# Optimization experiments

Measured on AMD Instinct MI355X. Metric: run time of the kernel, lower is better.

Reference implementation:

```python
import jax, jax.numpy as jnp
import numpy as np

# bitsandbytes NF4 codebook (16 levels, normalized to [-1, 1])
NF4_CODE = jnp.array([
    -1.0, -0.6961928009986877, -0.5250730514526367, -0.39491748809814453,
    -0.28444138169288635, -0.18477343022823334, -0.09105003625154495, 0.0,
    0.07958029955625534, 0.16093020141124725, 0.24611230194568634,
    0.33791524171829224, 0.44070982933044434, 0.5626170039176941,
    0.7229568362236023, 1.0], dtype=jnp.float32)

BLOCK = 64  # bitsandbytes default quantization blocksize
TOK, DIN, DOUT, RANK = 8192, 4096, 4096, 16
LORA_ALPHA = 16
SCALING = LORA_ALPHA / RANK ** 0.5  # rslora


def setup_inputs() -> dict:
    key = jax.random.key(0)
    k1, k2, k3, k4, k5, k6 = jax.random.split(key, 6)
    x = jax.random.normal(k1, (TOK, DIN), dtype=jnp.float32)
    w_codes = jax.random.randint(k2, (DOUT, DIN), 0, 16, dtype=jnp.int32)
    absmax = jax.random.uniform(k3, (DOUT, DIN // BLOCK), dtype=jnp.float32)
    bias = jax.random.normal(k4, (DOUT,), dtype=jnp.float32)
    lora_A = jax.random.normal(k5, (DIN, RANK), dtype=jnp.float32) * (1.0 / DIN ** 0.5)
    lora_B = jax.random.normal(k6, (RANK, DOUT), dtype=jnp.float32) * 0.02
    return {"x": x, "w_codes": w_codes, "absmax": absmax, "bias": bias,
            "lora_A": lora_A, "lora_B": lora_B}


def reference(x, w_codes, absmax, bias, lora_A, lora_B):
    # Dequantize NF4 base weight: codebook lookup * per-block absmax scale
    # W: [DOUT, DIN], absmax broadcast over blocks of 64 along DIN
    W = NF4_CODE[w_codes] * jnp.repeat(absmax, BLOCK, axis=1)
    base_out = x @ W.T + bias                      # [TOK, DOUT]
    lora_out = (x @ lora_A) @ lora_B               # low-rank path [TOK, DOUT]
    return base_out + lora_out * SCALING
```

## Files before the change

kernel.cpp:

```cpp
#include <hip/hip_runtime.h>
#include <hip/hip_bf16.h>
#include <cstdint>
#include <cstddef>

#define TOK   8192
#define DIN   4096
#define DOUT  4096
#define RANK  16
#define KE    4128

#define BM 256
#define BN 256
#define BKT 32
#define NKT (KE / BKT)
#define NBUF 3

typedef __attribute__((ext_vector_type(8))) short bf16x8;
typedef __attribute__((ext_vector_type(4))) float f32x4;
typedef __attribute__((ext_vector_type(8))) unsigned short u16x8;

__device__ __constant__ float NF4_CODE_D[16] = {
    -1.0f, -0.6961928009986877f, -0.5250730514526367f, -0.39491748809814453f,
    -0.28444138169288635f, -0.18477343022823334f, -0.09105003625154495f, 0.0f,
    0.07958029955625534f, 0.16093020141124725f, 0.24611230194568634f,
    0.33791524171829224f, 0.44070982933044434f, 0.5626170039176941f,
    0.7229568362236023f, 1.0f};

__device__ __forceinline__ unsigned short f2bf(float f) {
    union { float f; unsigned u; } v; v.f = f;
    unsigned u = v.u;
    unsigned r = (u + 0x7FFFu + ((u >> 16) & 1u)) >> 16;
    return (unsigned short)r;
}

__device__ __forceinline__ void async_copy16(const void* g, void* l) {
    __builtin_amdgcn_global_load_lds(
        (const __attribute__((address_space(1))) void*)g,
        (__attribute__((address_space(3))) void*)l,
        16, 0, 0);
}

__global__ __launch_bounds__(256) void prep_x(const float* __restrict__ x,
                                              const float* __restrict__ lora_A,
                                              unsigned short* __restrict__ xe) {
    const int tid = threadIdx.x;
    const int l = tid & 63;
    const int w = tid >> 6;
    const int t0 = blockIdx.x * 16 + w * 4;

    float p[4][16];
#pragma unroll
    for (int a = 0; a < 4; ++a)
#pragma unroll
        for (int r = 0; r < 16; ++r) p[a][r] = 0.f;

    for (int it = 0; it < 16; ++it) {
        const int kb = it * 256 + l * 4;
        float4 xv[4];
#pragma unroll
        for (int a = 0; a < 4; ++a)
            xv[a] = *(const float4*)(x + (size_t)(t0 + a) * DIN + kb);
#pragma unroll
        for (int a = 0; a < 4; ++a) {
            ushort4 s;
            s.x = f2bf(xv[a].x); s.y = f2bf(xv[a].y);
            s.z = f2bf(xv[a].z); s.w = f2bf(xv[a].w);
            *(ushort4*)(xe + (size_t)(t0 + a) * KE + kb) = s;
        }
#pragma unroll
        for (int j = 0; j < 4; ++j) {
            const float4* ap = (const float4*)(lora_A + (size_t)(kb + j) * RANK);
            const float4 a0 = ap[0], a1 = ap[1], a2 = ap[2], a3 = ap[3];
            const float av[16] = {a0.x, a0.y, a0.z, a0.w, a1.x, a1.y, a1.z, a1.w,
                                  a2.x, a2.y, a2.z, a2.w, a3.x, a3.y, a3.z, a3.w};
#pragma unroll
            for (int a = 0; a < 4; ++a) {
                const float xs = (j == 0) ? xv[a].x : (j == 1) ? xv[a].y
                                : (j == 2) ? xv[a].z : xv[a].w;
#pragma unroll
                for (int r = 0; r < 16; ++r) p[a][r] += xs * av[r];
            }
        }
    }

#pragma unroll
    for (int a = 0; a < 4; ++a) {
#pragma unroll
        for (int r = 0; r < 16; ++r) {
            float v = p[a][r];
#pragma unroll
            for (int off = 32; off > 0; off >>= 1) v += __shfl_xor(v, off, 64);
            if (l == r)
                xe[(size_t)(t0 + a) * KE + DIN + r] = f2bf(4.0f * v);
        }
        if (l >= 16 && l < 32)
            xe[(size_t)(t0 + a) * KE + DIN + l] =
                (l == 16) ? (unsigned short)0x3F80u : (unsigned short)0u;
    }
}

__global__ __launch_bounds__(256) void dequant_w(const int* __restrict__ codes,
                                                 const float* __restrict__ absmax,
                                                 unsigned short* __restrict__ we) {
    __shared__ float tab[16];
    if (threadIdx.x < 16) tab[threadIdx.x] = NF4_CODE_D[threadIdx.x];
    __syncthreads();
    const size_t tid = (size_t)blockIdx.x * 256 + threadIdx.x;
    const size_t base = tid * 8;
    const int o = (int)(base >> 12);
    const int k = (int)(base & (DIN - 1));
    const float am = absmax[base >> 6];
    const int4 c0 = *(const int4*)(codes + base);
    const int4 c1 = *(const int4*)(codes + base + 4);
    u16x8 ov;
    ov[0] = f2bf(tab[c0.x] * am);
    ov[1] = f2bf(tab[c0.y] * am);
    ov[2] = f2bf(tab[c0.z] * am);
    ov[3] = f2bf(tab[c0.w] * am);
    ov[4] = f2bf(tab[c1.x] * am);
    ov[5] = f2bf(tab[c1.y] * am);
    ov[6] = f2bf(tab[c1.z] * am);
    ov[7] = f2bf(tab[c1.w] * am);
    *(u16x8*)(we + (size_t)o * KE + k) = ov;
}

__global__ __launch_bounds__(256) void fill_wtail(const float* __restrict__ lora_B,
                                                  const float* __restrict__ bias,
                                                  unsigned short* __restrict__ we) {
    const int o = blockIdx.x * 256 + threadIdx.x;
    if (o >= DOUT) return;
    unsigned short* dst = we + (size_t)o * KE + DIN;
#pragma unroll
    for (int r = 0; r < RANK; ++r) dst[r] = f2bf(lora_B[(size_t)r * DOUT + o]);
    dst[16] = f2bf(bias[o]);
#pragma unroll
    for (int r = 17; r < 32; ++r) dst[r] = 0;
}

__global__ __launch_bounds__(512, 2) void gemm_bt(const unsigned short* __restrict__ A,
                                                  const unsigned short* __restrict__ B,
                                                  float* __restrict__ C) {
    __shared__ __attribute__((aligned(1024))) char smem[NBUF * 32768];

    const int tid = threadIdx.x;
    const int l = tid & 63;
    const int w = tid >> 6;
    const int wm = w >> 2;
    const int wn = w & 3;

    const int tm = blockIdx.x >> 4;
    const int tn = blockIdx.x & 15;
    const int rowBase = tm * BM;
    const int colBase = tn * BN;

    int srow[2], scolb[2], loffs[2];
#pragma unroll
    for (int g = 0; g < 2; ++g) {
        const int loff = g * 8192 + tid * 16;
        const int soff = loff ^ (((loff >> 7) & 7) << 4);
        loffs[g] = loff;
        srow[g] = soff >> 6;
        scolb[g] = soff & 63;
    }

    auto stage = [&](int t) {
        char* Ad = smem + (t % NBUF) * 32768;
        char* Bd = Ad + 16384;
        const int k0 = t * BKT;
#pragma unroll
        for (int g = 0; g < 2; ++g)
            async_copy16((const char*)A + ((size_t)(rowBase + srow[g]) * KE + k0) * 2 + scolb[g],
                         Ad + loffs[g]);
#pragma unroll
        for (int g = 0; g < 2; ++g)
            async_copy16((const char*)B + ((size_t)(colBase + srow[g]) * KE + k0) * 2 + scolb[g],
                         Bd + loffs[g]);
    };

    const int lmask = ((l >> 1) & 7) << 4;
    const int aoff = (((wm * 128 + (l & 15)) * 64) + ((l >> 4) * 16)) ^ lmask;
    const int boff = (((wn * 64 + (l & 15)) * 64) + ((l >> 4) * 16)) ^ lmask;

    f32x4 acc[8][4];
#pragma unroll
    for (int m = 0; m < 8; ++m)
#pragma unroll
        for (int n = 0; n < 4; ++n) acc[m][n] = (f32x4){0.f, 0.f, 0.f, 0.f};

    stage(0);
    stage(1);

    for (int t = 0; t < NKT; ++t) {
        if (t < NKT - 1) {
            asm volatile("s_waitcnt vmcnt(4)" ::: "memory");
        } else {
            asm volatile("s_waitcnt vmcnt(0)" ::: "memory");
        }
        __builtin_amdgcn_s_barrier();
        __builtin_amdgcn_sched_barrier(0);

        if (t + 2 < NKT) stage(t + 2);

        const char* At = smem + (t % NBUF) * 32768;
        const char* Bt = At + 16384;

        bf16x8 bfr[4];
#pragma unroll
        for (int n = 0; n < 4; ++n)
            bfr[n] = *(const bf16x8*)(Bt + boff + n * 1024);
#pragma unroll
        for (int m = 0; m < 8; ++m) {
            const bf16x8 af = *(const bf16x8*)(At + aoff + m * 1024);
#pragma unroll
            for (int n = 0; n < 4; ++n)
                acc[m][n] = __builtin_amdgcn_mfma_f32_16x16x32_bf16(
                    af, bfr[n], acc[m][n], 0, 0, 0);
        }
    }

#pragma unroll
    for (int m = 0; m < 8; ++m) {
        const int rowg = rowBase + wm * 128 + m * 16 + (l >> 4) * 4;
#pragma unroll
        for (int n = 0; n < 4; ++n) {
            const int colg = colBase + wn * 64 + n * 16 + (l & 15);
            float* cp = C + (size_t)rowg * DOUT + colg;
#pragma unroll
            for (int r = 0; r < 4; ++r) cp[(size_t)r * DOUT] = acc[m][n][r];
        }
    }
}

extern "C" void kernel_launch(void* const* d_in, const int* in_sizes, int n_in,
                              void* d_out, int out_size, void* d_ws, size_t ws_size,
                              hipStream_t stream) {
    const float* x      = (const float*)d_in[0];
    const int*   codes  = (const int*)d_in[1];
    const float* absmax = (const float*)d_in[2];
    const float* bias   = (const float*)d_in[3];
    const float* lora_A = (const float*)d_in[4];
    const float* lora_B = (const float*)d_in[5];
    float* out = (float*)d_out;

    unsigned short* xe = (unsigned short*)d_ws;
    unsigned short* we = xe + (size_t)TOK * KE;

    prep_x<<<TOK / 16, 256, 0, stream>>>(x, lora_A, xe);
    dequant_w<<<(DOUT * (size_t)DIN / 8) / 256, 256, 0, stream>>>(codes, absmax, we);
    fill_wtail<<<DOUT / 256, 256, 0, stream>>>(lora_B, bias, we);
    gemm_bt<<<(TOK / BM) * (DOUT / BN), 512, 0, stream>>>(xe, we, out);
}
```

Before: 375.5 us.

## Fuse prep kernels and shrink GEMM tile to 128x256 with double buffering

Merges the three preprocessing kernels (x conversion with LoRA-A projection, NF4 dequant, weight tail fill) into one launch dispatched by block index, which removes launch overhead. The GEMM tile shrinks from 256x256 to 128x256 with two LDS buffers instead of three, and launch bounds allow four blocks per CU, raising occupancy at the cost of more B-tile reloads. The K extension is padded from 4128 to 4160, and s_setprio is placed around the MFMA loop. The waitcnt is now vmcnt(0) with a prefetch depth of one stage, so less load latency is hidden per block.

Measured after the change: 394.0 us. +4.9%, slower.

```diff
diff --git a/kernel.cpp b/kernel.cpp
--- a/kernel.cpp
+++ b/kernel.cpp
@@ -7,13 +7,16 @@
 #define DIN   4096
 #define DOUT  4096
 #define RANK  16
-#define KE    4128
-
-#define BM 256
+#define KE    4160
+#define NT    (KE / 32)
+
+#define BM 128
 #define BN 256
-#define BKT 32
-#define NKT (KE / BKT)
-#define NBUF 3
+#define NBLK ((TOK / BM) * (DOUT / BN))
+
+#define PXB 512
+#define DQB 8192
+#define TLB 16
 
 typedef __attribute__((ext_vector_type(8))) short bf16x8;
 typedef __attribute__((ext_vector_type(4))) float f32x4;
@@ -40,107 +43,104 @@
         16, 0, 0);
 }
 
-__global__ __launch_bounds__(256) void prep_x(const float* __restrict__ x,
-                                              const float* __restrict__ lora_A,
-                                              unsigned short* __restrict__ xe) {
+__global__ __launch_bounds__(256) void prep_fused(
+        const float* __restrict__ x, const float* __restrict__ lora_A,
+        const int* __restrict__ codes, const float* __restrict__ absmax,
+        const float* __restrict__ bias, const float* __restrict__ lora_B,
+        unsigned short* __restrict__ xe, unsigned short* __restrict__ we) {
+    __shared__ float tab[16];
+    const int bid = blockIdx.x;
     const int tid = threadIdx.x;
-    const int l = tid & 63;
-    const int w = tid >> 6;
-    const int t0 = blockIdx.x * 16 + w * 4;
-
-    float p[4][16];
-#pragma unroll
-    for (int a = 0; a < 4; ++a)
-#pragma unroll
-        for (int r = 0; r < 16; ++r) p[a][r] = 0.f;
-
-    for (int it = 0; it < 16; ++it) {
-        const int kb = it * 256 + l * 4;
-        float4 xv[4];
+
+    if (bid < PXB) {
+        const int l = tid & 63;
+        const int w = tid >> 6;
+        const int t0 = bid * 16 + w * 4;
+
+        float p[4][16];
 #pragma unroll
         for (int a = 0; a < 4; ++a)
-            xv[a] = *(const float4*)(x + (size_t)(t0 + a) * DIN + kb);
+#pragma unroll
+            for (int r = 0; r < 16; ++r) p[a][r] = 0.f;
+
+        for (int it = 0; it < 16; ++it) {
+            const int kb = it * 256 + l * 4;
+            float4 xv[4];
+#pragma unroll
+            for (int a = 0; a < 4; ++a)
+                xv[a] = *(const float4*)(x + (size_t)(t0 + a) * DIN + kb);
+#pragma unroll
+            for (int a = 0; a < 4; ++a) {
+                ushort4 s;
+                s.x = f2bf(xv[a].x); s.y = f2bf(xv[a].y);
+                s.z = f2bf(xv[a].z); s.w = f2bf(xv[a].w);
+                *(ushort4*)(xe + (size_t)(t0 + a) * KE + kb) = s;
+            }
+#pragma unroll
+            for (int j = 0; j < 4; ++j) {
+                const float4* ap = (const float4*)(lora_A + (size_t)(kb + j) * RANK);
+                const float4 a0 = ap[0], a1 = ap[1], a2 = ap[2], a3 = ap[3];
+                const float av[16] = {a0.x, a0.y, a0.z, a0.w, a1.x, a1.y, a1.z, a1.w,
+                                      a2.x, a2.y, a2.z, a2.w, a3.x, a3.y, a3.z, a3.w};
+#pragma unroll
+                for (int a = 0; a < 4; ++a) {
+                    const float xs = (j == 0) ? xv[a].x : (j == 1) ? xv[a].y
+                                    : (j == 2) ? xv[a].z : xv[a].w;
+#pragma unroll
+                    for (int r = 0; r < 16; ++r) p[a][r] += xs * av[r];
+                }
+            }
+        }
+
 #pragma unroll
         for (int a = 0; a < 4; ++a) {
-            ushort4 s;
-            s.x = f2bf(xv[a].x); s.y = f2bf(xv[a].y);
-            s.z = f2bf(xv[a].z); s.w = f2bf(xv[a].w);
-            *(ushort4*)(xe + (size_t)(t0 + a) * KE + kb) = s;
-        }
-#pragma unroll
-        for (int j = 0; j < 4; ++j) {
-            const float4* ap = (const float4*)(lora_A + (size_t)(kb + j) * RANK);
-            const float4 a0 = ap[0], a1 = ap[1], a2 = ap[2], a3 = ap[3];
-            const float av[16] = {a0.x, a0.y, a0.z, a0.w, a1.x, a1.y, a1.z, a1.w,
-                                  a2.x, a2.y, a2.z, a2.w, a3.x, a3.y, a3.z, a3.w};
-#pragma unroll
-            for (int a = 0; a < 4; ++a) {
-                const float xs = (j == 0) ? xv[a].x : (j == 1) ? xv[a].y
-                                : (j == 2) ? xv[a].z : xv[a].w;
-#pragma unroll
-                for (int r = 0; r < 16; ++r) p[a][r] += xs * av[r];
+#pragma unroll
+            for (int r = 0; r < 16; ++r) {
+                float v = p[a][r];
+#pragma unroll
+                for (int off = 32; off > 0; off >>= 1) v += __shfl_xor(v, off, 64);
+                if (l == r)
+                    xe[(size_t)(t0 + a) * KE + DIN + r] = f2bf(4.0f * v);
             }
-        }
-    }
-
-#pragma unroll
-    for (int a = 0; a < 4; ++a) {
-#pragma unroll
-        for (int r = 0; r < 16; ++r) {
-            float v = p[a][r];
-#pragma unroll
-            for (int off = 32; off > 0; off >>= 1) v += __shfl_xor(v, off, 64);
-            if (l == r)
-                xe[(size_t)(t0 + a) * KE + DIN + r] = f2bf(4.0f * v);
-        }
-        if (l >= 16 && l < 32)
-            xe[(size_t)(t0 + a) * KE + DIN + l] =
-                (l == 16) ? (unsigned short)0x3F80u : (unsigned short)0u;
-    }
-}
-
-__global__ __launch_bounds__(256) void dequant_w(const int* __restrict__ codes,
-                                                 const float* __restrict__ absmax,
-                                                 unsigned short* __restrict__ we) {
-    __shared__ float tab[16];
-    if (threadIdx.x < 16) tab[threadIdx.x] = NF4_CODE_D[threadIdx.x];
-    __syncthreads();
-    const size_t tid = (size_t)blockIdx.x * 256 + threadIdx.x;
-    const size_t base = tid * 8;
-    const int o = (int)(base >> 12);
-    const int k = (int)(base & (DIN - 1));
-    const float am = absmax[base >> 6];
-    const int4 c0 = *(const int4*)(codes + base);
-    const int4 c1 = *(const int4*)(codes + base + 4);
-    u16x8 ov;
-    ov[0] = f2bf(tab[c0.x] * am);
-    ov[1] = f2bf(tab[c0.y] * am);
-    ov[2] = f2bf(tab[c0.z] * am);
-    ov[3] = f2bf(tab[c0.w] * am);
-    ov[4] = f2bf(tab[c1.x] * am);
-    ov[5] = f2bf(tab[c1.y] * am);
-    ov[6] = f2bf(tab[c1.z] * am);
-    ov[7] = f2bf(tab[c1.w] * am);
-    *(u16x8*)(we + (size_t)o * KE + k) = ov;
-}
-
-__global__ __launch_bounds__(256) void fill_wtail(const float* __restrict__ lora_B,
-                                                  const float* __restrict__ bias,
-                                                  unsigned short* __restrict__ we) {
-    const int o = blockIdx.x * 256 + threadIdx.x;
-    if (o >= DOUT) return;
-    unsigned short* dst = we + (size_t)o * KE + DIN;
-#pragma unroll
-    for (int r = 0; r < RANK; ++r) dst[r] = f2bf(lora_B[(size_t)r * DOUT + o]);
-    dst[16] = f2bf(bias[o]);
-#pragma unroll
-    for (int r = 17; r < 32; ++r) dst[r] = 0;
-}
-
-__global__ __launch_bounds__(512, 2) void gemm_bt(const unsigned short* __restrict__ A,
+            if (l >= 16)
+                xe[(size_t)(t0 + a) * KE + DIN + l] =
+                    (l == 16) ? (unsigned short)0x3F80u : (unsigned short)0u;
+        }
+    } else if (bid < PXB + DQB) {
+        if (tid < 16) tab[tid] = NF4_CODE_D[tid];
+        __syncthreads();
+        const size_t t = (size_t)(bid - PXB) * 256 + tid;
+        const size_t base = t * 8;
+        const int o = (int)(base >> 12);
+        const int k = (int)(base & (DIN - 1));
+        const float am = absmax[base >> 6];
+        const int4 c0 = *(const int4*)(codes + base);
+        const int4 c1 = *(const int4*)(codes + base + 4);
+        u16x8 ov;
+        ov[0] = f2bf(tab[c0.x] * am);
+        ov[1] = f2bf(tab[c0.y] * am);
+        ov[2] = f2bf(tab[c0.z] * am);
+        ov[3] = f2bf(tab[c0.w] * am);
+        ov[4] = f2bf(tab[c1.x] * am);
+        ov[5] = f2bf(tab[c1.y] * am);
+        ov[6] = f2bf(tab[c1.z] * am);
+        ov[7] = f2bf(tab[c1.w] * am);
+        *(u16x8*)(we + (size_t)o * KE + k) = ov;
+    } else {
+        const int o = (bid - PXB - DQB) * 256 + tid;
+        unsigned short* dst = we + (size_t)o * KE + DIN;
+#pragma unroll
+        for (int r = 0; r < RANK; ++r) dst[r] = f2bf(lora_B[(size_t)r * DOUT + o]);
+        dst[16] = f2bf(bias[o]);
+#pragma unroll
+        for (int r = 17; r < 64; ++r) dst[r] = 0;
+    }
+}
+
+__global__ __launch_bounds__(512, 4) void gemm_bt(const unsigned short* __restrict__ A,
                                                   const unsigned short* __restrict__ B,
                                                   float* __restrict__ C) {
-    __shared__ __attribute__((aligned(1024))) char smem[NBUF * 32768];
+    __shared__ __attribute__((aligned(1024))) char smem[2 * 24576];
 
     const int tid = threadIdx.x;
     const int l = tid & 63;
@@ -153,77 +153,79 @@
     const int rowBase = tm * BM;
     const int colBase = tn * BN;
 
-    int srow[2], scolb[2], loffs[2];
+    int aRow, aColB;
+    {
+        const int loff = tid * 16;
+        const int soff = loff ^ (((loff >> 7) & 7) << 4);
+        aRow = soff >> 6; aColB = soff & 63;
+    }
+    int bRow[2], bColB[2];
 #pragma unroll
     for (int g = 0; g < 2; ++g) {
         const int loff = g * 8192 + tid * 16;
         const int soff = loff ^ (((loff >> 7) & 7) << 4);
-        loffs[g] = loff;
-        srow[g] = soff >> 6;
-        scolb[g] = soff & 63;
+        bRow[g] = soff >> 6; bColB[g] = soff & 63;
     }
 
     auto stage = [&](int t) {
-        char* Ad = smem + (t % NBUF) * 32768;
-        char* Bd = Ad + 16384;
-        const int k0 = t * BKT;
+        char* dst = smem + (t & 1) * 24576;
+        const int k0 = t * 32;
+        async_copy16((const char*)A + ((size_t)(rowBase + aRow) * KE + k0) * 2 + aColB,
+                     dst + tid * 16);
 #pragma unroll
         for (int g = 0; g < 2; ++g)
-            async_copy16((const char*)A + ((size_t)(rowBase + srow[g]) * KE + k0) * 2 + scolb[g],
-                         Ad + loffs[g]);
-#pragma unroll
-        for (int g = 0; g < 2; ++g)
-            async_copy16((const char*)B + ((size_t)(colBase + srow[g]) * KE + k0) * 2 + scolb[g],
-                         Bd + loffs[g]);
+            async_copy16((const char*)B + ((size_t)(colBase + bRow[g]) * KE + k0) * 2 + bColB[g],
+                         dst + 8192 + g * 8192 + tid * 16);
     };
 
+    const int lr = l & 15;
+    const int lk16 = (l >> 4) * 16;
     const int lmask = ((l >> 1) & 7) << 4;
-    const int aoff = (((wm * 128 + (l & 15)) * 64) + ((l >> 4) * 16)) ^ lmask;
-    const int boff = (((wn * 64 + (l & 15)) * 64) + ((l >> 4) * 16)) ^ lmask;
-
-    f32x4 acc[8][4];
-#pragma unroll
-    for (int m = 0; m < 8; ++m)
+    int aoff[4], boff[4];
+#pragma unroll
+    for (int m = 0; m < 4; ++m)
+        aoff[m] = (((wm * 64 + m * 16 + lr) * 64) + lk16) ^ lmask;
+#pragma unroll
+    for (int n = 0; n < 4; ++n)
+        boff[n] = 8192 + ((((wn * 64 + n * 16 + lr) * 64) + lk16) ^ lmask);
+
+    f32x4 acc[4][4];
+#pragma unroll
+    for (int m = 0; m < 4; ++m)
 #pragma unroll
         for (int n = 0; n < 4; ++n) acc[m][n] = (f32x4){0.f, 0.f, 0.f, 0.f};
 
     stage(0);
-    stage(1);
-
-    for (int t = 0; t < NKT; ++t) {
-        if (t < NKT - 1) {
-            asm volatile("s_waitcnt vmcnt(4)" ::: "memory");
-        } else {
-            asm volatile("s_waitcnt vmcnt(0)" ::: "memory");
-        }
+
+    for (int t = 0; t < NT; ++t) {
+        asm volatile("s_waitcnt vmcnt(0)" ::: "memory");
         __builtin_amdgcn_s_barrier();
         __builtin_amdgcn_sched_barrier(0);
-
-        if (t + 2 < NKT) stage(t + 2);
-
-        const char* At = smem + (t % NBUF) * 32768;
-        const char* Bt = At + 16384;
-
+        if (t + 1 < NT) stage(t + 1);
+
+        const char* S = smem + (t & 1) * 24576;
         bf16x8 bfr[4];
 #pragma unroll
         for (int n = 0; n < 4; ++n)
-            bfr[n] = *(const bf16x8*)(Bt + boff + n * 1024);
-#pragma unroll
-        for (int m = 0; m < 8; ++m) {
-            const bf16x8 af = *(const bf16x8*)(At + aoff + m * 1024);
+            bfr[n] = *(const bf16x8*)(S + boff[n]);
+        __builtin_amdgcn_s_setprio(1);
+#pragma unroll
+        for (int m = 0; m < 4; ++m) {
+            const bf16x8 af = *(const bf16x8*)(S + aoff[m]);
 #pragma unroll
             for (int n = 0; n < 4; ++n)
                 acc[m][n] = __builtin_amdgcn_mfma_f32_16x16x32_bf16(
                     af, bfr[n], acc[m][n], 0, 0, 0);
         }
-    }
-
-#pragma unroll
-    for (int m = 0; m < 8; ++m) {
-        const int rowg = rowBase + wm * 128 + m * 16 + (l >> 4) * 4;
+        __builtin_amdgcn_s_setprio(0);
+    }
+
+#pragma unroll
+    for (int m = 0; m < 4; ++m) {
+        const int rowg = rowBase + wm * 64 + m * 16 + (l >> 4) * 4;
 #pragma unroll
         for (int n = 0; n < 4; ++n) {
-            const int colg = colBase + wn * 64 + n * 16 + (l & 15);
+            const int colg = colBase + wn * 64 + n * 16 + lr;
             float* cp = C + (size_t)rowg * DOUT + colg;
 #pragma unroll
             for (int r = 0; r < 4; ++r) cp[(size_t)r * DOUT] = acc[m][n][r];
@@ -245,8 +247,7 @@
     unsigned short* xe = (unsigned short*)d_ws;
     unsigned short* we = xe + (size_t)TOK * KE;
 
-    prep_x<<<TOK / 16, 256, 0, stream>>>(x, lora_A, xe);
-    dequant_w<<<(DOUT * (size_t)DIN / 8) / 256, 256, 0, stream>>>(codes, absmax, we);
-    fill_wtail<<<DOUT / 256, 256, 0, stream>>>(lora_B, bias, we);
-    gemm_bt<<<(TOK / BM) * (DOUT / BN), 512, 0, stream>>>(xe, we, out);
-}
+    prep_fused<<<PXB + DQB + TLB, 256, 0, stream>>>(x, lora_A, codes, absmax,
+                                                    bias, lora_B, xe, we);
+    gemm_bt<<<NBLK, 512, 0, stream>>>(xe, we, out);
+}
```
